# Performance work log

Hardware: AMD Instinct MI355X
Metric: run time of the kernel (lower is better)

Reference implementation:

```python
import jax, jax.numpy as jnp
import numpy as np

STATE_DIM = 128
NUM_STATES = 16
BATCH = 16384


def setup_inputs() -> dict:
    key = jax.random.key(0)
    k1, k2, k3, k4 = jax.random.split(key, 4)
    x = jax.random.normal(k1, (BATCH, STATE_DIM), dtype=jnp.float32)
    state_idx = jax.random.randint(k2, (BATCH,), 0, NUM_STATES)
    A_all = jax.random.normal(k3, (NUM_STATES, STATE_DIM, STATE_DIM), dtype=jnp.float32)
    C_all = jax.random.normal(k4, (NUM_STATES, STATE_DIM, STATE_DIM), dtype=jnp.float32)
    return {"x": x, "state_idx": state_idx, "A_all": A_all, "C_all": C_all}


def reference(x, state_idx, A_all, C_all):
    # Per-sample expert matrix gather: [B, D, D]
    Ag = A_all[state_idx]
    Cg = C_all[state_idx]
    # state = relu(x @ A_i) per sample, batched via einsum
    state = jax.nn.relu(jnp.einsum('bd,bde->be', x, Ag))
    # observation = state @ C_i
    out = jnp.einsum('be,bef->bf', state, Cg)
    return out
```

## Files before the change

### kernel.cpp

```cpp
#include <hip/hip_runtime.h>

#define D 128
#define NS 16
#define BATCH 16384
#define TILE 64
#define CHUNK 512
#define PST 40

typedef __attribute__((ext_vector_type(8))) short short8;
typedef __attribute__((ext_vector_type(4))) float f32x4;

__device__ __forceinline__ unsigned short f2bf(float f) {
  unsigned u = __builtin_bit_cast(unsigned, f);
  u += 0x7FFFu + ((u >> 16) & 1u);
  return (unsigned short)(u >> 16);
}

__device__ __forceinline__ uint4 pack8(float4 a, float4 b) {
  unsigned short p[8];
  p[0] = f2bf(a.x); p[1] = f2bf(a.y); p[2] = f2bf(a.z); p[3] = f2bf(a.w);
  p[4] = f2bf(b.x); p[5] = f2bf(b.y); p[6] = f2bf(b.z); p[7] = f2bf(b.w);
  return *(const uint4*)p;
}

__global__ __launch_bounds__(256, 2) void prep_weights(
    const float* __restrict__ A_all, const float* __restrict__ C_all,
    unsigned short* __restrict__ Wt) {
  __shared__ unsigned short T[D * PST];
  const int b = blockIdx.x;
  const int s = b >> 3, mat = (b >> 2) & 1, r0 = (b & 3) * 32;
  const float* __restrict__ src =
      (mat ? C_all : A_all) + (size_t)s * D * D + (size_t)r0 * D;
  unsigned short* __restrict__ dst = Wt + (size_t)(mat * NS + s) * D * D + r0;
  const int t = threadIdx.x;
  {
    const int r = t >> 3, c0 = (t & 7) * 16;
    const float4* srow = (const float4*)(src + r * D + c0);
#pragma unroll
    for (int i = 0; i < 4; i++) {
      float4 v = srow[i];
      T[(c0 + i * 4 + 0) * PST + r] = f2bf(v.x);
      T[(c0 + i * 4 + 1) * PST + r] = f2bf(v.y);
      T[(c0 + i * 4 + 2) * PST + r] = f2bf(v.z);
      T[(c0 + i * 4 + 3) * PST + r] = f2bf(v.w);
    }
  }
  __syncthreads();
  {
    const int c = t >> 1, rh = (t & 1) * 16;
    const uint4* tsrc = (const uint4*)&T[c * PST + rh];
    uint4* d4 = (uint4*)(dst + (size_t)c * D + rh);
    d4[0] = tsrc[0];
    d4[1] = tsrc[1];
  }
}

__global__ __launch_bounds__(256, 2) void ssm_mfma(
    const float* __restrict__ x,
    const int* __restrict__ sidx,
    const unsigned short* __restrict__ Wt,
    float* __restrict__ out) {
  __shared__ unsigned short XH[TILE * D];
  __shared__ int rowlist[CHUNK];
  __shared__ int wcnt[8];

  const int b = blockIdx.x;
  const int s = (b & 7) | (((b >> 3) & 1) << 3);
  const int c0 = (b >> 4) * CHUNK;
  const int tid = threadIdx.x;
  const int lane = tid & 63, w = tid >> 6;
  const int l15 = lane & 15, quad = lane >> 4;

  const int v0 = sidx[c0 + tid];
  const int v1 = sidx[c0 + 256 + tid];

  short8 aW[4][2], cW[4][2];
  {
    const unsigned short* As =
        Wt + (size_t)s * D * D + (w * 32 + l15) * D + quad * 8;
    const unsigned short* Cs = As + NS * D * D;
#pragma unroll
    for (int kb = 0; kb < 4; kb++)
#pragma unroll
      for (int nb = 0; nb < 2; nb++) {
        aW[kb][nb] = *(const short8*)(As + nb * 16 * D + kb * 32);
        cW[kb][nb] = *(const short8*)(Cs + nb * 16 * D + kb * 32);
      }
  }

  const unsigned long long lanelt = (1ull << lane) - 1ull;
  const unsigned long long m0 = __ballot(v0 == s);
  const unsigned long long m1 = __ballot(v1 == s);
  if (lane == 0) { wcnt[w] = (int)__popcll(m0); wcnt[4 + w] = (int)__popcll(m1); }
  __syncthreads();
  int pre0 = 0, pre1 = 0, tot0 = 0, cnt = 0;
#pragma unroll
  for (int ww = 0; ww < 4; ww++) {
    if (ww < w) { pre0 += wcnt[ww]; pre1 += wcnt[4 + ww]; }
    tot0 += wcnt[ww];
    cnt += wcnt[ww] + wcnt[4 + ww];
  }
  if (v0 == s) rowlist[pre0 + (int)__popcll(m0 & lanelt)] = c0 + tid;
  if (v1 == s) rowlist[tot0 + pre1 + (int)__popcll(m1 & lanelt)] = c0 + 256 + tid;
  if (cnt == 0) return;

#pragma unroll 1
  for (int i0 = 0; i0 < cnt; i0 += TILE) {
    __syncthreads();

    {
      const int r = tid >> 2, q4 = tid & 3;
      const int rid = (i0 + r < cnt) ? rowlist[i0 + r] : -1;
      if (rid >= 0) {
        const float4* src = (const float4*)(x + (size_t)rid * D + q4 * 32);
#pragma unroll
        for (int i = 0; i < 4; i++) {
          float4 va = src[2 * i];
          float4 vb = src[2 * i + 1];
          *(uint4*)&XH[r * D + (((q4 * 4 + i) ^ (r & 15)) << 3)] = pack8(va, vb);
        }
      } else {
        uint4 z = {0, 0, 0, 0};
#pragma unroll
        for (int i = 0; i < 4; i++)
          *(uint4*)&XH[r * D + (((q4 * 4 + i) ^ (r & 15)) << 3)] = z;
      }
    }
    __syncthreads();

    f32x4 acc[4][2];
#pragma unroll
    for (int ti = 0; ti < 4; ti++) {
      acc[ti][0] = (f32x4){0.f, 0.f, 0.f, 0.f};
      acc[ti][1] = (f32x4){0.f, 0.f, 0.f, 0.f};
    }
#pragma unroll
    for (int kb = 0; kb < 4; kb++) {
      short8 aF[4];
#pragma unroll
      for (int ti = 0; ti < 4; ti++)
        aF[ti] = *(const short8*)&XH[(ti * 16 + l15) * D +
                                     (((kb * 4 + quad) ^ l15) << 3)];
#pragma unroll
      for (int ti = 0; ti < 4; ti++) {
        acc[ti][0] = __builtin_amdgcn_mfma_f32_16x16x32_bf16(aF[ti], aW[kb][0],
                                                             acc[ti][0], 0, 0, 0);
        acc[ti][1] = __builtin_amdgcn_mfma_f32_16x16x32_bf16(aF[ti], aW[kb][1],
                                                             acc[ti][1], 0, 0, 0);
      }
    }
    __syncthreads();

#pragma unroll
    for (int ti = 0; ti < 4; ti++)
#pragma unroll
      for (int nb = 0; nb < 2; nb++)
#pragma unroll
        for (int rr = 0; rr < 4; rr++) {
          float v = acc[ti][nb][rr];
          const int row = ti * 16 + quad * 4 + rr;
          const int ch = (w * 4 + nb * 2 + (l15 >> 3)) ^ (quad * 4 + rr);
          XH[row * D + (ch << 3) + (l15 & 7)] = f2bf(v > 0.f ? v : 0.f);
        }
    __syncthreads();

#pragma unroll
    for (int ti = 0; ti < 4; ti++) {
      acc[ti][0] = (f32x4){0.f, 0.f, 0.f, 0.f};
      acc[ti][1] = (f32x4){0.f, 0.f, 0.f, 0.f};
    }
#pragma unroll
    for (int kb = 0; kb < 4; kb++) {
      short8 aF[4];
#pragma unroll
      for (int ti = 0; ti < 4; ti++)
        aF[ti] = *(const short8*)&XH[(ti * 16 + l15) * D +
                                     (((kb * 4 + quad) ^ l15) << 3)];
#pragma unroll
      for (int ti = 0; ti < 4; ti++) {
        acc[ti][0] = __builtin_amdgcn_mfma_f32_16x16x32_bf16(aF[ti], cW[kb][0],
                                                             acc[ti][0], 0, 0, 0);
        acc[ti][1] = __builtin_amdgcn_mfma_f32_16x16x32_bf16(aF[ti], cW[kb][1],
                                                             acc[ti][1], 0, 0, 0);
      }
    }

#pragma unroll
    for (int ti = 0; ti < 4; ti++)
#pragma unroll
      for (int rr = 0; rr < 4; rr++) {
        const int rl = ti * 16 + quad * 4 + rr;
        if (i0 + rl < cnt) {
          float* orow = out + (size_t)rowlist[i0 + rl] * D + w * 32 + l15;
          orow[0] = acc[ti][0][rr];
          orow[16] = acc[ti][1][rr];
        }
      }
  }
}

extern "C" void kernel_launch(void* const* d_in, const int* in_sizes, int n_in,
                              void* d_out, int out_size, void* d_ws, size_t ws_size,
                              hipStream_t stream) {
  const float* x = (const float*)d_in[0];
  const int* sidx = (const int*)d_in[1];
  const float* A_all = (const float*)d_in[2];
  const float* C_all = (const float*)d_in[3];
  float* out = (float*)d_out;

  unsigned short* Wt = (unsigned short*)d_ws;

  prep_weights<<<128, 256, 0, stream>>>(A_all, C_all, Wt);
  ssm_mfma<<<512, 256, 0, stream>>>(x, sidx, Wt, out);
}
```

Before: 74.81 us.

## Halve chunk/tile size, load x directly into MFMA fragments, defer C weights

Halves the per-block chunk of samples and the row tile, doubling the grid to 1024 blocks and raising the launch-bounds occupancy target. The first GEMM now reads x straight from global memory into MFMA operand registers with bf16 conversion, dropping the LDS staging pass and its barrier. C weights are loaded inside the loop after the first GEMM instead of being held in registers for the whole kernel, to lower register pressure. In exchange, each wave now loads the x rows itself, so global reads of x are duplicated across the four waves, and C weights are refetched on every tile.

```diff
diff --git a/kernel.cpp b/kernel.cpp
--- a/kernel.cpp
+++ b/kernel.cpp
@@ -3,8 +3,8 @@
 #define D 128
 #define NS 16
 #define BATCH 16384
-#define TILE 64
-#define CHUNK 512
+#define CHUNK 256
+#define TILE 32
 #define PST 40
 
 typedef __attribute__((ext_vector_type(8))) short short8;
@@ -16,11 +16,11 @@
   return (unsigned short)(u >> 16);
 }
 
-__device__ __forceinline__ uint4 pack8(float4 a, float4 b) {
+__device__ __forceinline__ short8 pack8s(float4 a, float4 b) {
   unsigned short p[8];
   p[0] = f2bf(a.x); p[1] = f2bf(a.y); p[2] = f2bf(a.z); p[3] = f2bf(a.w);
   p[4] = f2bf(b.x); p[5] = f2bf(b.y); p[6] = f2bf(b.z); p[7] = f2bf(b.w);
-  return *(const uint4*)p;
+  return *(const short8*)p;
 }
 
 __global__ __launch_bounds__(256, 2) void prep_weights(
@@ -55,14 +55,14 @@
   }
 }
 
-__global__ __launch_bounds__(256, 2) void ssm_mfma(
+__global__ __launch_bounds__(256, 4) void ssm_mfma(
     const float* __restrict__ x,
     const int* __restrict__ sidx,
     const unsigned short* __restrict__ Wt,
     float* __restrict__ out) {
-  __shared__ unsigned short XH[TILE * D];
+  __shared__ unsigned short H[TILE * D];
   __shared__ int rowlist[CHUNK];
-  __shared__ int wcnt[8];
+  __shared__ int wcnt[4];
 
   const int b = blockIdx.x;
   const int s = (b & 7) | (((b >> 3) & 1) << 3);
@@ -72,87 +72,75 @@
   const int l15 = lane & 15, quad = lane >> 4;
 
   const int v0 = sidx[c0 + tid];
-  const int v1 = sidx[c0 + 256 + tid];
-
-  short8 aW[4][2], cW[4][2];
-  {
-    const unsigned short* As =
-        Wt + (size_t)s * D * D + (w * 32 + l15) * D + quad * 8;
-    const unsigned short* Cs = As + NS * D * D;
-#pragma unroll
-    for (int kb = 0; kb < 4; kb++)
-#pragma unroll
-      for (int nb = 0; nb < 2; nb++) {
-        aW[kb][nb] = *(const short8*)(As + nb * 16 * D + kb * 32);
-        cW[kb][nb] = *(const short8*)(Cs + nb * 16 * D + kb * 32);
-      }
-  }
+
+  const unsigned short* As =
+      Wt + (size_t)s * D * D + (size_t)(w * 32 + l15) * D + quad * 8;
+  short8 aW[4][2];
+#pragma unroll
+  for (int kb = 0; kb < 4; kb++)
+#pragma unroll
+    for (int nb = 0; nb < 2; nb++)
+      aW[kb][nb] = *(const short8*)(As + nb * 16 * D + kb * 32);
 
   const unsigned long long lanelt = (1ull << lane) - 1ull;
   const unsigned long long m0 = __ballot(v0 == s);
-  const unsigned long long m1 = __ballot(v1 == s);
-  if (lane == 0) { wcnt[w] = (int)__popcll(m0); wcnt[4 + w] = (int)__popcll(m1); }
+  if (lane == 0) wcnt[w] = (int)__popcll(m0);
   __syncthreads();
-  int pre0 = 0, pre1 = 0, tot0 = 0, cnt = 0;
+  int pre = 0, cnt = 0;
 #pragma unroll
   for (int ww = 0; ww < 4; ww++) {
-    if (ww < w) { pre0 += wcnt[ww]; pre1 += wcnt[4 + ww]; }
-    tot0 += wcnt[ww];
-    cnt += wcnt[ww] + wcnt[4 + ww];
-  }
-  if (v0 == s) rowlist[pre0 + (int)__popcll(m0 & lanelt)] = c0 + tid;
-  if (v1 == s) rowlist[tot0 + pre1 + (int)__popcll(m1 & lanelt)] = c0 + 256 + tid;
+    if (ww < w) pre += wcnt[ww];
+    cnt += wcnt[ww];
+  }
+  if (v0 == s) rowlist[pre + (int)__popcll(m0 & lanelt)] = c0 + tid;
   if (cnt == 0) return;
 
 #pragma unroll 1
   for (int i0 = 0; i0 < cnt; i0 += TILE) {
     __syncthreads();
 
+    const int r0i = i0 + l15, r1i = i0 + 16 + l15;
+    const int rid0 = (r0i < cnt) ? rowlist[r0i] : -1;
+    const int rid1 = (r1i < cnt) ? rowlist[r1i] : -1;
+
+    f32x4 acc[2][2];
+#pragma unroll
+    for (int ti = 0; ti < 2; ti++)
+#pragma unroll
+      for (int nb = 0; nb < 2; nb++) acc[ti][nb] = (f32x4){0.f, 0.f, 0.f, 0.f};
+#pragma unroll
+    for (int kb = 0; kb < 4; kb++) {
+      short8 a0 = {0, 0, 0, 0, 0, 0, 0, 0};
+      short8 a1 = {0, 0, 0, 0, 0, 0, 0, 0};
+      if (rid0 >= 0) {
+        const float4* p = (const float4*)(x + (size_t)rid0 * D + kb * 32 + quad * 8);
+        a0 = pack8s(p[0], p[1]);
+      }
+      if (rid1 >= 0) {
+        const float4* p = (const float4*)(x + (size_t)rid1 * D + kb * 32 + quad * 8);
+        a1 = pack8s(p[0], p[1]);
+      }
+#pragma unroll
+      for (int nb = 0; nb < 2; nb++) {
+        acc[0][nb] = __builtin_amdgcn_mfma_f32_16x16x32_bf16(a0, aW[kb][nb],
+                                                             acc[0][nb], 0, 0, 0);
+        acc[1][nb] = __builtin_amdgcn_mfma_f32_16x16x32_bf16(a1, aW[kb][nb],
+                                                             acc[1][nb], 0, 0, 0);
+      }
+    }
+
+    short8 cW[4][2];
     {
-      const int r = tid >> 2, q4 = tid & 3;
-      const int rid = (i0 + r < cnt) ? rowlist[i0 + r] : -1;
-      if (rid >= 0) {
-        const float4* src = (const float4*)(x + (size_t)rid * D + q4 * 32);
-#pragma unroll
-        for (int i = 0; i < 4; i++) {
-          float4 va = src[2 * i];
-          float4 vb = src[2 * i + 1];
-          *(uint4*)&XH[r * D + (((q4 * 4 + i) ^ (r & 15)) << 3)] = pack8(va, vb);
-        }
-      } else {
-        uint4 z = {0, 0, 0, 0};
-#pragma unroll
-        for (int i = 0; i < 4; i++)
-          *(uint4*)&XH[r * D + (((q4 * 4 + i) ^ (r & 15)) << 3)] = z;
-      }
-    }
-    __syncthreads();
-
-    f32x4 acc[4][2];
-#pragma unroll
-    for (int ti = 0; ti < 4; ti++) {
-      acc[ti][0] = (f32x4){0.f, 0.f, 0.f, 0.f};
-      acc[ti][1] = (f32x4){0.f, 0.f, 0.f, 0.f};
-    }
-#pragma unroll
-    for (int kb = 0; kb < 4; kb++) {
-      short8 aF[4];
-#pragma unroll
-      for (int ti = 0; ti < 4; ti++)
-        aF[ti] = *(const short8*)&XH[(ti * 16 + l15) * D +
-                                     (((kb * 4 + quad) ^ l15) << 3)];
-#pragma unroll
-      for (int ti = 0; ti < 4; ti++) {
-        acc[ti][0] = __builtin_amdgcn_mfma_f32_16x16x32_bf16(aF[ti], aW[kb][0],
-                                                             acc[ti][0], 0, 0, 0);
-        acc[ti][1] = __builtin_amdgcn_mfma_f32_16x16x32_bf16(aF[ti], aW[kb][1],
-                                                             acc[ti][1], 0, 0, 0);
-      }
-    }
-    __syncthreads();
-
-#pragma unroll
-    for (int ti = 0; ti < 4; ti++)
+      const unsigned short* Cs = As + (size_t)NS * D * D;
+#pragma unroll
+      for (int kb = 0; kb < 4; kb++)
+#pragma unroll
+        for (int nb = 0; nb < 2; nb++)
+          cW[kb][nb] = *(const short8*)(Cs + nb * 16 * D + kb * 32);
+    }
+
+#pragma unroll
+    for (int ti = 0; ti < 2; ti++)
 #pragma unroll
       for (int nb = 0; nb < 2; nb++)
 #pragma unroll
@@ -160,24 +148,23 @@
           float v = acc[ti][nb][rr];
           const int row = ti * 16 + quad * 4 + rr;
           const int ch = (w * 4 + nb * 2 + (l15 >> 3)) ^ (quad * 4 + rr);
-          XH[row * D + (ch << 3) + (l15 & 7)] = f2bf(v > 0.f ? v : 0.f);
+          H[row * D + (ch << 3) + (l15 & 7)] = f2bf(v > 0.f ? v : 0.f);
         }
     __syncthreads();
 
 #pragma unroll
-    for (int ti = 0; ti < 4; ti++) {
-      acc[ti][0] = (f32x4){0.f, 0.f, 0.f, 0.f};
-      acc[ti][1] = (f32x4){0.f, 0.f, 0.f, 0.f};
-    }
+    for (int ti = 0; ti < 2; ti++)
+#pragma unroll
+      for (int nb = 0; nb < 2; nb++) acc[ti][nb] = (f32x4){0.f, 0.f, 0.f, 0.f};
 #pragma unroll
     for (int kb = 0; kb < 4; kb++) {
-      short8 aF[4];
-#pragma unroll
-      for (int ti = 0; ti < 4; ti++)
-        aF[ti] = *(const short8*)&XH[(ti * 16 + l15) * D +
-                                     (((kb * 4 + quad) ^ l15) << 3)];
-#pragma unroll
-      for (int ti = 0; ti < 4; ti++) {
+      short8 aF[2];
+#pragma unroll
+      for (int ti = 0; ti < 2; ti++)
+        aF[ti] = *(const short8*)&H[(ti * 16 + l15) * D +
+                                    (((kb * 4 + quad) ^ l15) << 3)];
+#pragma unroll
+      for (int ti = 0; ti < 2; ti++) {
         acc[ti][0] = __builtin_amdgcn_mfma_f32_16x16x32_bf16(aF[ti], cW[kb][0],
                                                              acc[ti][0], 0, 0, 0);
         acc[ti][1] = __builtin_amdgcn_mfma_f32_16x16x32_bf16(aF[ti], cW[kb][1],
@@ -186,12 +173,12 @@
     }
 
 #pragma unroll
-    for (int ti = 0; ti < 4; ti++)
+    for (int ti = 0; ti < 2; ti++)
 #pragma unroll
       for (int rr = 0; rr < 4; rr++) {
-        const int rl = ti * 16 + quad * 4 + rr;
-        if (i0 + rl < cnt) {
-          float* orow = out + (size_t)rowlist[i0 + rl] * D + w * 32 + l15;
+        const int rl = i0 + ti * 16 + quad * 4 + rr;
+        if (rl < cnt) {
+          float* orow = out + (size_t)rowlist[rl] * D + w * 32 + l15;
           orow[0] = acc[ti][0][rr];
           orow[16] = acc[ti][1][rr];
         }
@@ -211,5 +198,5 @@
   unsigned short* Wt = (unsigned short*)d_ws;
 
   prep_weights<<<128, 256, 0, stream>>>(A_all, C_all, Wt);
-  ssm_mfma<<<512, 256, 0, stream>>>(x, sidx, Wt, out);
-}
+  ssm_mfma<<<BATCH / CHUNK * NS, 256, 0, stream>>>(x, sidx, Wt, out);
+}
```

Result: slower. 82.01 us (+9.6%).
